# Kernel optimization log

Measured on AMD Instinct MI355X. Metric: run time of the kernel, lower is better.

The kernel has to match this reference:

```python
import jax, jax.numpy as jnp
import numpy as np

BN_EPS = 1e-5

def _bn(x, g, b):
    # BatchNorm1d, training-mode batch statistics
    mu = x.mean(axis=0)
    var = x.var(axis=0)
    return g * (x - mu) / jnp.sqrt(var + BN_EPS) + b

def setup_inputs() -> dict:
    key = jax.random.key(0)
    ks = jax.random.split(key, 10)
    B2, D_in, D1, DIMS, C = 16384, 1024, 512, 256, 40
    B = B2 // 2
    def w(k, shape, fan_in):
        return jax.random.normal(k, shape, jnp.float32) / np.float32(np.sqrt(fan_in))
    return {
        "lufeat": jax.random.normal(ks[0], (B2, D_in), jnp.float32),
        "llabel": jax.random.randint(ks[1], (B,), 0, C),
        "W1": w(ks[2], (D_in, D1), D_in), "b1": jnp.zeros(D1, jnp.float32),
        "W2": w(ks[3], (D1, DIMS), D1), "b2": jnp.zeros(DIMS, jnp.float32),
        "W3": w(ks[4], (DIMS + C, 256), DIMS + C), "b3": jnp.zeros(256, jnp.float32),
        "W4": w(ks[5], (256, 64), 256), "b4": jnp.zeros(64, jnp.float32),
        "W5": w(ks[6], (64, 1), 64), "b5": jnp.zeros(1, jnp.float32),
        "g1": jnp.ones(256, jnp.float32), "be1": jnp.zeros(256, jnp.float32),
        "g2": jnp.ones(64, jnp.float32), "be2": jnp.zeros(64, jnp.float32),
        "mbank0": jax.random.normal(ks[7], (C, DIMS), jnp.float32),
        "start0": jnp.zeros(C, jnp.float32),
    }

def reference(lufeat, llabel, W1, b1, W2, b2, W3, b3, W4, b4, W5, b5,
              g1, be1, g2, be2, mbank0, start0):
    B = lufeat.shape[0] // 2
    h = (lufeat @ W1 + b1) @ W2 + b2            # [2B, dims]
    h = h / jnp.linalg.norm(h, axis=1, keepdims=True)
    lfeat, ufeat = h[:B], h[B:]

    # Sequential per-sample memory-bank scatter/EMA update (detached feats)
    lf_sg = jax.lax.stop_gradient(lfeat)
    def step(carry, xs):
        start, mbank = carry
        lab, feat = xs
        row = jnp.where(start[lab] == 0, feat, 0.9 * mbank[lab] + 0.1 * feat)
        return (start.at[lab].set(1.0), mbank.at[lab].set(row)), None
    (_, mbank), _ = jax.lax.scan(step, (start0, mbank0), (llabel, lf_sg))
    mbank = jax.lax.stop_gradient(mbank)

    # cdist retrieval: [B, C] euclidean distances
    lm = jnp.linalg.norm(lfeat[:, None, :] - mbank[None, :, :], axis=-1)
    lscores = lm.min(axis=-1)
    um = jnp.linalg.norm(ufeat[:, None, :] - mbank[None, :, :], axis=-1)

    uf = jnp.concatenate([ufeat, um], axis=-1)   # [B, dims + C]
    u = jax.nn.relu(_bn(uf @ W3 + b3, g1, be1))
    u = jax.nn.relu(_bn(u @ W4 + b4, g2, be2))   # dropout = identity (eval)
    uscores = u @ W5 + b5                        # [B, 1]
    return lscores, uscores, mbank
```

## Files before the change

kernel.cpp:

```cpp
#include <hip/hip_runtime.h>
#include <hip/hip_bf16.h>
#include <stdint.h>

typedef __attribute__((ext_vector_type(4))) float f32x4;
typedef __attribute__((ext_vector_type(8))) short s16x8;
typedef __attribute__((ext_vector_type(4))) unsigned short u16x4;
typedef __attribute__((ext_vector_type(4))) int i32x4;

#define B2T 16384
#define BH 8192
#define DIN 1024
#define DD1 512
#define DIMS 256
#define NC 40
#define CAPS 2048

__device__ __forceinline__ unsigned short f2b(float f) {
  unsigned int u = __builtin_bit_cast(unsigned int, f);
  u += 0x7FFFu + ((u >> 16) & 1u);
  return (unsigned short)(u >> 16);
}

__global__ __launch_bounds__(256) void prep_weff(const float* __restrict__ W1,
                                                 const float* __restrict__ W2,
                                                 unsigned short* __restrict__ WeffT) {
  __shared__ float W1s[32][33];
  __shared__ float W2s[32][33];
  int t = threadIdx.x;
  int k0 = blockIdx.x * 32, n0 = blockIdx.y * 32;
  int nn = t & 31, kq = t >> 5;
  float acc[4] = {0.f, 0.f, 0.f, 0.f};
  for (int j0 = 0; j0 < DD1; j0 += 32) {
#pragma unroll
    for (int i = 0; i < 4; ++i) {
      int idx = t + 256 * i;
      int kk = idx >> 5, jj = idx & 31;
      W1s[kk][jj] = W1[(size_t)(k0 + kk) * DD1 + j0 + jj];
      W2s[kk][jj] = W2[(size_t)(j0 + kk) * DIMS + n0 + jj];
    }
    __syncthreads();
#pragma unroll
    for (int jj = 0; jj < 32; ++jj) {
      float w2v = W2s[jj][nn];
#pragma unroll
      for (int q = 0; q < 4; ++q) acc[q] += W1s[kq * 4 + q][jj] * w2v;
    }
    __syncthreads();
  }
  u16x4 pk;
#pragma unroll
  for (int q = 0; q < 4; ++q) pk[q] = f2b(acc[q]);
  *(u16x4*)(WeffT + (size_t)(n0 + nn) * DIN + k0 + kq * 4) = pk;
}

__global__ __launch_bounds__(256) void prep_misc(const float* __restrict__ b1,
                                                 const float* __restrict__ W2,
                                                 const float* __restrict__ b2,
                                                 const float* __restrict__ W3,
                                                 const float* __restrict__ W4,
                                                 float* __restrict__ beff,
                                                 unsigned short* __restrict__ W3T,
                                                 unsigned short* __restrict__ W4T) {
  int b = blockIdx.x, t = threadIdx.x;
  if (b == 0) {
    float a0 = 0.f, a1 = 0.f, a2 = 0.f, a3 = 0.f, a4 = 0.f, a5 = 0.f, a6 = 0.f, a7 = 0.f;
    for (int j = 0; j < DD1; j += 8) {
      a0 += b1[j + 0] * W2[(size_t)(j + 0) * DIMS + t];
      a1 += b1[j + 1] * W2[(size_t)(j + 1) * DIMS + t];
      a2 += b1[j + 2] * W2[(size_t)(j + 2) * DIMS + t];
      a3 += b1[j + 3] * W2[(size_t)(j + 3) * DIMS + t];
      a4 += b1[j + 4] * W2[(size_t)(j + 4) * DIMS + t];
      a5 += b1[j + 5] * W2[(size_t)(j + 5) * DIMS + t];
      a6 += b1[j + 6] * W2[(size_t)(j + 6) * DIMS + t];
      a7 += b1[j + 7] * W2[(size_t)(j + 7) * DIMS + t];
    }
    beff[t] = b2[t] + (((a0 + a1) + (a2 + a3)) + ((a4 + a5) + (a6 + a7)));
  } else if (b <= 320) {
    int idx = (b - 1) * 256 + t;
    int n = idx / 320, k = idx - n * 320;
    float v = (k < 296) ? W3[(size_t)k * 256 + n] : 0.0f;
    W3T[(size_t)n * 320 + k] = f2b(v);
  } else {
    int idx = (b - 321) * 256 + t;
    int n = idx >> 8, k = idx & 255;
    W4T[(size_t)n * 256 + k] = f2b(W4[(size_t)k * 64 + n]);
  }
}

template <int AMODE, int NB, int MI, int CW, int EPI>
__global__ __launch_bounds__(256) void gemm_core(
    const void* __restrict__ Aptr, int lda, const unsigned short* __restrict__ BT,
    const float* __restrict__ bias, float* __restrict__ C, int ldc, int K,
    float* __restrict__ sums, float* __restrict__ ssqs,
    const float* __restrict__ bnsum, const float* __restrict__ bnssq,
    const float* __restrict__ bng, const float* __restrict__ bnbe,
    unsigned short* __restrict__ uf) {
  constexpr int AR = (4 / CW) * MI * 16;
  __shared__ short A_s[AR][72];
  __shared__ short B_s[NB][72];
  __shared__ float rs[4][AR];
  int t = threadIdx.x;
  int m0 = blockIdx.x * AR;
  int w = t >> 6, lane = t & 63, q = lane >> 4, ln = lane & 15;
  f32x4 acc[MI][4];
#pragma unroll
  for (int mi = 0; mi < MI; ++mi)
#pragma unroll
    for (int ni = 0; ni < 4; ++ni) acc[mi][ni] = (f32x4){0.f, 0.f, 0.f, 0.f};

  for (int kk = 0; kk < K; kk += 64) {
    if constexpr (AMODE == 0 || AMODE == 2) {
      const float* A = (const float*)Aptr;
#pragma unroll
      for (int i = 0; i < AR / 32; ++i) {
        int ch = t + 256 * i;
        int row = ch >> 3, kp = (ch & 7) * 8;
        const f32x4* src = (const f32x4*)(A + (size_t)(m0 + row) * lda + kk + kp);
        f32x4 v0 = src[0], v1 = src[1];
        if constexpr (AMODE == 2) {
          float vv[8] = {v0[0], v0[1], v0[2], v0[3], v1[0], v1[1], v1[2], v1[3]};
#pragma unroll
          for (int j = 0; j < 8; ++j) {
            int f = kk + kp + j;
            float mu = bnsum[f] * (1.0f / 8192.0f);
            float var = bnssq[f] * (1.0f / 8192.0f) - mu * mu;
            float sc = bng[f] * rsqrtf(var + 1e-5f);
            float sh = bnbe[f] - mu * sc;
            vv[j] = fmaxf(vv[j] * sc + sh, 0.0f);
          }
          v0 = (f32x4){vv[0], vv[1], vv[2], vv[3]};
          v1 = (f32x4){vv[4], vv[5], vv[6], vv[7]};
        }
        s16x8 p;
        p[0] = (short)f2b(v0[0]); p[1] = (short)f2b(v0[1]);
        p[2] = (short)f2b(v0[2]); p[3] = (short)f2b(v0[3]);
        p[4] = (short)f2b(v1[0]); p[5] = (short)f2b(v1[1]);
        p[6] = (short)f2b(v1[2]); p[7] = (short)f2b(v1[3]);
        *(s16x8*)&A_s[row][kp] = p;
      }
    } else {
      const unsigned short* A = (const unsigned short*)Aptr;
#pragma unroll
      for (int i = 0; i < AR / 32; ++i) {
        int ch = t + 256 * i;
        int row = ch >> 3, kp = (ch & 7) * 8;
        *(s16x8*)&A_s[row][kp] = *(const s16x8*)(A + (size_t)(m0 + row) * lda + kk + kp);
      }
    }
#pragma unroll
    for (int i = 0; i < NB * 8 / 256; ++i) {
      int ch = t + 256 * i;
      int n = ch >> 3, kp = (ch & 7) * 8;
      *(s16x8*)&B_s[n][kp] = *(const s16x8*)(BT + (size_t)n * K + kk + kp);
    }
    __syncthreads();
#pragma unroll
    for (int k32 = 0; k32 < 64; k32 += 32) {
      s16x8 af[MI];
      int ab = (w / CW) * MI * 16;
#pragma unroll
      for (int mi = 0; mi < MI; ++mi)
        af[mi] = *(const s16x8*)&A_s[ab + mi * 16 + ln][k32 + q * 8];
      int nb0 = (w % CW) * 64;
#pragma unroll
      for (int ni = 0; ni < 4; ++ni) {
        s16x8 bfr = *(const s16x8*)&B_s[nb0 + ni * 16 + ln][k32 + q * 8];
#pragma unroll
        for (int mi = 0; mi < MI; ++mi)
          acc[mi][ni] = __builtin_amdgcn_mfma_f32_16x16x32_bf16(af[mi], bfr, acc[mi][ni], 0, 0, 0);
      }
    }
    __syncthreads();
  }

  float v[MI][4][4];
#pragma unroll
  for (int mi = 0; mi < MI; ++mi)
#pragma unroll
    for (int ni = 0; ni < 4; ++ni) {
      float bv = bias[(w % CW) * 64 + ni * 16 + ln];
#pragma unroll
      for (int r = 0; r < 4; ++r) v[mi][ni][r] = acc[mi][ni][r] + bv;
    }

  if constexpr (EPI == 1) {
    float p[MI][4];
#pragma unroll
    for (int mi = 0; mi < MI; ++mi)
#pragma unroll
      for (int r = 0; r < 4; ++r) {
        float s = v[mi][0][r] * v[mi][0][r] + v[mi][1][r] * v[mi][1][r] +
                  v[mi][2][r] * v[mi][2][r] + v[mi][3][r] * v[mi][3][r];
        s += __shfl_xor(s, 1); s += __shfl_xor(s, 2);
        s += __shfl_xor(s, 4); s += __shfl_xor(s, 8);
        p[mi][r] = s;
      }
    if (ln == 0) {
#pragma unroll
      for (int mi = 0; mi < MI; ++mi)
#pragma unroll
        for (int r = 0; r < 4; ++r) rs[w][mi * 16 + q * 4 + r] = p[mi][r];
    }
    __syncthreads();
    if (t < AR) rs[0][t] = rsqrtf(rs[0][t] + rs[1][t] + rs[2][t] + rs[3][t]);
    __syncthreads();
#pragma unroll
    for (int mi = 0; mi < MI; ++mi)
#pragma unroll
      for (int r = 0; r < 4; ++r) {
        int rib = mi * 16 + q * 4 + r;
        float inv = rs[0][rib];
        int grow = m0 + rib;
#pragma unroll
        for (int ni = 0; ni < 4; ++ni) {
          int col = w * 64 + ni * 16 + ln;
          float nv = v[mi][ni][r] * inv;
          C[(size_t)grow * ldc + col] = nv;
          if (grow >= BH) uf[(size_t)(grow - BH) * 320 + col] = f2b(nv);
        }
      }
  } else {
#pragma unroll
    for (int mi = 0; mi < MI; ++mi)
#pragma unroll
      for (int ni = 0; ni < 4; ++ni)
#pragma unroll
        for (int r = 0; r < 4; ++r) {
          int grow = m0 + (w / CW) * MI * 16 + mi * 16 + q * 4 + r;
          int col = (w % CW) * 64 + ni * 16 + ln;
          C[(size_t)grow * ldc + col] = v[mi][ni][r];
        }
    if constexpr (EPI == 2 || EPI == 3) {
#pragma unroll
      for (int ni = 0; ni < 4; ++ni) {
        float s = 0.f, s2 = 0.f;
#pragma unroll
        for (int mi = 0; mi < MI; ++mi)
#pragma unroll
          for (int r = 0; r < 4; ++r) {
            float x = v[mi][ni][r];
            s += x; s2 += x * x;
          }
        s += __shfl_xor(s, 16); s += __shfl_xor(s, 32);
        s2 += __shfl_xor(s2, 16); s2 += __shfl_xor(s2, 32);
        if (q == 0) {
          int col = (w % CW) * 64 + ni * 16 + ln;
          atomicAdd(&sums[col], s);
          atomicAdd(&ssqs[col], s2);
        }
      }
    }
  }
}

__global__ __launch_bounds__(256) void bank_kernel(const int* __restrict__ llabel,
                                                   const float* __restrict__ Hn,
                                                   const float* __restrict__ mbank0,
                                                   const float* __restrict__ start0,
                                                   float* __restrict__ mbank_out,
                                                   float* __restrict__ msq) {
  __shared__ i32x4 lab4[BH / 4];
  __shared__ int idx_s[CAPS];
  __shared__ int wcnt[4];
  __shared__ float red[4];
  int t = threadIdx.x, c = blockIdx.x;
  int w = t >> 6, lane = t & 63;

  for (int i = t; i < BH / 4; i += 256) lab4[i] = ((const i32x4*)llabel)[i];
  __syncthreads();
  const int* lab_s = (const int*)lab4;

  int base0 = w * (BH / 4);
  int cnt = 0;
  for (int b = 0; b < BH / 4; b += 64)
    cnt += (int)__popcll(__ballot(lab_s[base0 + b + lane] == c));
  if (lane == 0) wcnt[w] = cnt;
  __syncthreads();
  int off = 0;
#pragma unroll
  for (int i = 0; i < 4; ++i)
    if (i < w) off += wcnt[i];
  int Ktot = wcnt[0] + wcnt[1] + wcnt[2] + wcnt[3];

  int running = off;
  for (int b = 0; b < BH / 4; b += 64) {
    bool hit = lab_s[base0 + b + lane] == c;
    unsigned long long mk = __ballot(hit);
    if (hit) {
      int pos = running + (int)__popcll(mk & ((1ull << lane) - 1ull));
      if (pos < CAPS) idx_s[pos] = base0 + b + lane;
    }
    running += (int)__popcll(mk);
  }
  __syncthreads();
  int K = Ktot < CAPS ? Ktot : CAPS;

  const float l09 = -0.15200309344504997f;
  bool fresh = (start0[c] == 0.0f);
  float out;
  if (K == 0) {
    out = mbank0[(size_t)c * DIMS + t];
  } else {
    float a0 = 0.f, a1 = 0.f, a2 = 0.f, a3 = 0.f, a4 = 0.f, a5 = 0.f, a6 = 0.f, a7 = 0.f;
    float w0fold = fresh ? exp2f((float)K * l09) : 0.f;
    int m = 0;
    for (; m + 8 <= K; m += 8) {
      float e = (float)(K - 1 - m);
      float wa = 0.1f * exp2f(e * l09) + (m == 0 ? w0fold : 0.f);
      a0 += wa * Hn[(size_t)idx_s[m + 0] * DIMS + t];
      a1 += 0.1f * exp2f((e - 1.f) * l09) * Hn[(size_t)idx_s[m + 1] * DIMS + t];
      a2 += 0.1f * exp2f((e - 2.f) * l09) * Hn[(size_t)idx_s[m + 2] * DIMS + t];
      a3 += 0.1f * exp2f((e - 3.f) * l09) * Hn[(size_t)idx_s[m + 3] * DIMS + t];
      a4 += 0.1f * exp2f((e - 4.f) * l09) * Hn[(size_t)idx_s[m + 4] * DIMS + t];
      a5 += 0.1f * exp2f((e - 5.f) * l09) * Hn[(size_t)idx_s[m + 5] * DIMS + t];
      a6 += 0.1f * exp2f((e - 6.f) * l09) * Hn[(size_t)idx_s[m + 6] * DIMS + t];
      a7 += 0.1f * exp2f((e - 7.f) * l09) * Hn[(size_t)idx_s[m + 7] * DIMS + t];
    }
    for (; m < K; ++m) {
      float wa = 0.1f * exp2f((float)(K - 1 - m) * l09) + (m == 0 ? w0fold : 0.f);
      a0 += wa * Hn[(size_t)idx_s[m] * DIMS + t];
    }
    float acc = ((a0 + a1) + (a2 + a3)) + ((a4 + a5) + (a6 + a7));
    float base_v = fresh ? 0.f : exp2f((float)K * l09) * mbank0[(size_t)c * DIMS + t];
    out = acc + base_v;
  }
  mbank_out[(size_t)c * DIMS + t] = out;
  float vv = out * out;
#pragma unroll
  for (int o = 32; o; o >>= 1) vv += __shfl_xor(vv, o);
  if ((t & 63) == 0) red[t >> 6] = vv;
  __syncthreads();
  if (t == 0) msq[c] = (red[0] + red[1]) + (red[2] + red[3]);
}

__global__ __launch_bounds__(128) void dist_kernel(const float* __restrict__ Hn,
                                                   const float* __restrict__ mbank,
                                                   const float* __restrict__ msq,
                                                   float* __restrict__ lscores,
                                                   unsigned short* __restrict__ uf) {
  __shared__ float Ms[NC][260];
  __shared__ float Hs[16][260];
  __shared__ float msq_s[NC];
  int t = threadIdx.x;
  int r0 = blockIdx.x * 16;
  for (int i = 0; i < NC; ++i) {
    Ms[i][t] = mbank[(size_t)i * DIMS + t];
    Ms[i][t + 128] = mbank[(size_t)i * DIMS + t + 128];
  }
  for (int i = 0; i < 16; ++i) {
    Hs[i][t] = Hn[(size_t)(r0 + i) * DIMS + t];
    Hs[i][t + 128] = Hn[(size_t)(r0 + i) * DIMS + t + 128];
  }
  if (t < NC) msq_s[t] = msq[t];
  __syncthreads();
  int r = t >> 3, c0 = (t & 7) * 5;
  float g0 = 0, g1 = 0, g2 = 0, g3 = 0, g4 = 0;
  for (int d = 0; d < DIMS; d += 4) {
    f32x4 f = *(const f32x4*)&Hs[r][d];
    f32x4 m0v = *(const f32x4*)&Ms[c0 + 0][d];
    f32x4 m1v = *(const f32x4*)&Ms[c0 + 1][d];
    f32x4 m2v = *(const f32x4*)&Ms[c0 + 2][d];
    f32x4 m3v = *(const f32x4*)&Ms[c0 + 3][d];
    f32x4 m4v = *(const f32x4*)&Ms[c0 + 4][d];
    g0 += f[0] * m0v[0] + f[1] * m0v[1] + f[2] * m0v[2] + f[3] * m0v[3];
    g1 += f[0] * m1v[0] + f[1] * m1v[1] + f[2] * m1v[2] + f[3] * m1v[3];
    g2 += f[0] * m2v[0] + f[1] * m2v[1] + f[2] * m2v[2] + f[3] * m2v[3];
    g3 += f[0] * m3v[0] + f[1] * m3v[1] + f[2] * m3v[2] + f[3] * m3v[3];
    g4 += f[0] * m4v[0] + f[1] * m4v[1] + f[2] * m4v[2] + f[3] * m4v[3];
  }
  int row = r0 + r;
  float d2[5];
  d2[0] = 1.0f + msq_s[c0 + 0] - 2.0f * g0;
  d2[1] = 1.0f + msq_s[c0 + 1] - 2.0f * g1;
  d2[2] = 1.0f + msq_s[c0 + 2] - 2.0f * g2;
  d2[3] = 1.0f + msq_s[c0 + 3] - 2.0f * g3;
  d2[4] = 1.0f + msq_s[c0 + 4] - 2.0f * g4;
  if (row < BH) {
    float mn = fminf(fminf(fminf(d2[0], d2[1]), fminf(d2[2], d2[3])), d2[4]);
    mn = fminf(mn, __shfl_xor(mn, 1, 8));
    mn = fminf(mn, __shfl_xor(mn, 2, 8));
    mn = fminf(mn, __shfl_xor(mn, 4, 8));
    if ((t & 7) == 0) lscores[row] = sqrtf(fmaxf(mn, 0.0f));
  } else {
    unsigned short* dst = uf + (size_t)(row - BH) * 320 + 256 + c0;
#pragma unroll
    for (int qq = 0; qq < 5; ++qq) dst[qq] = f2b(sqrtf(fmaxf(d2[qq], 0.0f)));
  }
}

__global__ __launch_bounds__(256) void uscore_bn(const float* __restrict__ y2,
                                                 const float* __restrict__ sums2,
                                                 const float* __restrict__ ssqs2,
                                                 const float* __restrict__ g2,
                                                 const float* __restrict__ be2,
                                                 const float* __restrict__ W5,
                                                 const float* __restrict__ b5,
                                                 float* __restrict__ out) {
  int t = threadIdx.x;
  int wv = t >> 6, lane = t & 63;
  int row = blockIdx.x * 4 + wv;
  float mu = sums2[lane] * (1.0f / 8192.0f);
  float var = ssqs2[lane] * (1.0f / 8192.0f) - mu * mu;
  float sc = g2[lane] * rsqrtf(var + 1e-5f);
  float sh = be2[lane] - mu * sc;
  float v = fmaxf(y2[(size_t)row * 64 + lane] * sc + sh, 0.0f) * W5[lane];
#pragma unroll
  for (int o = 32; o; o >>= 1) v += __shfl_xor(v, o);
  if (lane == 0) out[row] = v + b5[0];
}

extern "C" void kernel_launch(void* const* d_in, const int* in_sizes, int n_in,
                              void* d_out, int out_size, void* d_ws, size_t ws_size,
                              hipStream_t stream) {
  const float* lufeat = (const float*)d_in[0];
  const int* llabel = (const int*)d_in[1];
  const float* W1 = (const float*)d_in[2];
  const float* b1 = (const float*)d_in[3];
  const float* W2 = (const float*)d_in[4];
  const float* b2 = (const float*)d_in[5];
  const float* W3 = (const float*)d_in[6];
  const float* b3 = (const float*)d_in[7];
  const float* W4 = (const float*)d_in[8];
  const float* b4 = (const float*)d_in[9];
  const float* W5 = (const float*)d_in[10];
  const float* b5 = (const float*)d_in[11];
  const float* g1 = (const float*)d_in[12];
  const float* be1 = (const float*)d_in[13];
  const float* g2 = (const float*)d_in[14];
  const float* be2 = (const float*)d_in[15];
  const float* mbank0 = (const float*)d_in[16];
  const float* start0 = (const float*)d_in[17];

  char* ws = (char*)d_ws;
  unsigned short* WeffT = (unsigned short*)(ws + 0);
  float* Hraw = (float*)(ws + 524288);
  float* ybuf = (float*)(ws + 524288);
  float* y2 = (float*)(ws + 8912896);
  unsigned short* uf = (unsigned short*)(ws + 17301504);
  unsigned short* W3T = (unsigned short*)(ws + 22544384);
  unsigned short* W4T = (unsigned short*)(ws + 22708224);
  float* beff = (float*)(ws + 22740992);
  float* sums1 = (float*)(ws + 22742016);
  float* ssq1 = sums1 + 256;
  float* sums2 = ssq1 + 256;
  float* ssq2 = sums2 + 64;
  float* msq = (float*)(ws + 22744576);

  float* lscores = (float*)d_out;
  float* uscores = lscores + 8192;
  float* mbank = uscores + 8192;

  hipMemsetAsync(sums1, 0, (256 + 256 + 64 + 64) * sizeof(float), stream);

  prep_weff<<<dim3(32, 8), 256, 0, stream>>>(W1, W2, WeffT);
  prep_misc<<<385, 256, 0, stream>>>(b1, W2, b2, W3, W4, beff, W3T, W4T);
  gemm_core<0, 256, 2, 4, 1><<<512, 256, 0, stream>>>(
      lufeat, 1024, WeffT, beff, Hraw, 256, 1024,
      nullptr, nullptr, nullptr, nullptr, nullptr, nullptr, uf);
  bank_kernel<<<NC, 256, 0, stream>>>(llabel, Hraw, mbank0, start0, mbank, msq);
  dist_kernel<<<1024, 128, 0, stream>>>(Hraw, mbank, msq, lscores, uf);
  gemm_core<1, 256, 2, 4, 2><<<256, 256, 0, stream>>>(
      uf, 320, W3T, b3, ybuf, 256, 320,
      sums1, ssq1, nullptr, nullptr, nullptr, nullptr, nullptr);
  gemm_core<2, 64, 1, 1, 3><<<128, 256, 0, stream>>>(
      ybuf, 256, W4T, b4, y2, 64, 256,
      sums2, ssq2, sums1, ssq1, g1, be1, nullptr);
  uscore_bn<<<2048, 256, 0, stream>>>(y2, sums2, ssq2, g2, be2, W5, b5, uscores);
}
```

Before: 264.2 us.

## Merge prep kernels and memset into one launch; double dist_kernel rows per block

Folds prep_weff, prep_misc and the stats memset into a single prep_all launch, which removes two launches and a memset. The W1·W2 product now stores W2 transposed in shared memory so the inner loop can use float4 LDS reads. dist_kernel switches to 256 threads handling 32 rows per block, which halves the grid and spreads the mbank staging over more rows. The visible compute indexing (r = t>>3) may need matching changes in the hidden part of the kernel.

New measurement: 244.4 us. -7.5%, faster.

```diff
diff --git a/kernel.cpp b/kernel.cpp
--- a/kernel.cpp
+++ b/kernel.cpp
@@ -21,48 +21,50 @@
   return (unsigned short)(u >> 16);
 }
 
-__global__ __launch_bounds__(256) void prep_weff(const float* __restrict__ W1,
-                                                 const float* __restrict__ W2,
-                                                 unsigned short* __restrict__ WeffT) {
-  __shared__ float W1s[32][33];
-  __shared__ float W2s[32][33];
-  int t = threadIdx.x;
-  int k0 = blockIdx.x * 32, n0 = blockIdx.y * 32;
-  int nn = t & 31, kq = t >> 5;
-  float acc[4] = {0.f, 0.f, 0.f, 0.f};
-  for (int j0 = 0; j0 < DD1; j0 += 32) {
-#pragma unroll
-    for (int i = 0; i < 4; ++i) {
-      int idx = t + 256 * i;
-      int kk = idx >> 5, jj = idx & 31;
-      W1s[kk][jj] = W1[(size_t)(k0 + kk) * DD1 + j0 + jj];
-      W2s[kk][jj] = W2[(size_t)(j0 + kk) * DIMS + n0 + jj];
-    }
-    __syncthreads();
-#pragma unroll
-    for (int jj = 0; jj < 32; ++jj) {
-      float w2v = W2s[jj][nn];
-#pragma unroll
-      for (int q = 0; q < 4; ++q) acc[q] += W1s[kq * 4 + q][jj] * w2v;
-    }
-    __syncthreads();
-  }
-  u16x4 pk;
-#pragma unroll
-  for (int q = 0; q < 4; ++q) pk[q] = f2b(acc[q]);
-  *(u16x4*)(WeffT + (size_t)(n0 + nn) * DIN + k0 + kq * 4) = pk;
-}
-
-__global__ __launch_bounds__(256) void prep_misc(const float* __restrict__ b1,
-                                                 const float* __restrict__ W2,
-                                                 const float* __restrict__ b2,
-                                                 const float* __restrict__ W3,
-                                                 const float* __restrict__ W4,
-                                                 float* __restrict__ beff,
-                                                 unsigned short* __restrict__ W3T,
-                                                 unsigned short* __restrict__ W4T) {
+__global__ __launch_bounds__(256) void prep_all(const float* __restrict__ W1,
+                                                const float* __restrict__ W2,
+                                                const float* __restrict__ b1,
+                                                const float* __restrict__ b2,
+                                                const float* __restrict__ W3,
+                                                const float* __restrict__ W4,
+                                                unsigned short* __restrict__ WeffT,
+                                                float* __restrict__ beff,
+                                                unsigned short* __restrict__ W3T,
+                                                unsigned short* __restrict__ W4T,
+                                                float* __restrict__ statz) {
+  __shared__ float W1s[32][36];
+  __shared__ float W2sT[32][36];
   int b = blockIdx.x, t = threadIdx.x;
-  if (b == 0) {
+  if (b < 256) {
+    int k0 = (b & 31) * 32, n0 = (b >> 5) * 32;
+    int nn = t & 31, kq = t >> 5;
+    f32x4 acc = (f32x4){0.f, 0.f, 0.f, 0.f};
+    for (int j0 = 0; j0 < DD1; j0 += 32) {
+#pragma unroll
+      for (int i = 0; i < 4; ++i) {
+        int idx = t + 256 * i;
+        int kk = idx >> 5, jj = idx & 31;
+        W1s[kk][jj] = W1[(size_t)(k0 + kk) * DD1 + j0 + jj];
+        W2sT[jj][kk] = W2[(size_t)(j0 + kk) * DIMS + n0 + jj];
+      }
+      __syncthreads();
+#pragma unroll
+      for (int jj4 = 0; jj4 < 8; ++jj4) {
+        f32x4 w2 = *(const f32x4*)&W2sT[nn][jj4 * 4];
+        f32x4 w1_0 = *(const f32x4*)&W1s[kq * 4 + 0][jj4 * 4];
+        f32x4 w1_1 = *(const f32x4*)&W1s[kq * 4 + 1][jj4 * 4];
+        f32x4 w1_2 = *(const f32x4*)&W1s[kq * 4 + 2][jj4 * 4];
+        f32x4 w1_3 = *(const f32x4*)&W1s[kq * 4 + 3][jj4 * 4];
+        acc[0] += w1_0[0] * w2[0] + w1_0[1] * w2[1] + w1_0[2] * w2[2] + w1_0[3] * w2[3];
+        acc[1] += w1_1[0] * w2[0] + w1_1[1] * w2[1] + w1_1[2] * w2[2] + w1_1[3] * w2[3];
+        acc[2] += w1_2[0] * w2[0] + w1_2[1] * w2[1] + w1_2[2] * w2[2] + w1_2[3] * w2[3];
+        acc[3] += w1_3[0] * w2[0] + w1_3[1] * w2[1] + w1_3[2] * w2[2] + w1_3[3] * w2[3];
+      }
+      __syncthreads();
+    }
+    u16x4 pk = {f2b(acc[0]), f2b(acc[1]), f2b(acc[2]), f2b(acc[3])};
+    *(u16x4*)(WeffT + (size_t)(n0 + nn) * DIN + k0 + kq * 4) = pk;
+  } else if (b == 256) {
     float a0 = 0.f, a1 = 0.f, a2 = 0.f, a3 = 0.f, a4 = 0.f, a5 = 0.f, a6 = 0.f, a7 = 0.f;
     for (int j = 0; j < DD1; j += 8) {
       a0 += b1[j + 0] * W2[(size_t)(j + 0) * DIMS + t];
@@ -75,15 +77,17 @@
       a7 += b1[j + 7] * W2[(size_t)(j + 7) * DIMS + t];
     }
     beff[t] = b2[t] + (((a0 + a1) + (a2 + a3)) + ((a4 + a5) + (a6 + a7)));
-  } else if (b <= 320) {
-    int idx = (b - 1) * 256 + t;
+  } else if (b < 577) {
+    int idx = (b - 257) * 256 + t;
     int n = idx / 320, k = idx - n * 320;
     float v = (k < 296) ? W3[(size_t)k * 256 + n] : 0.0f;
     W3T[(size_t)n * 320 + k] = f2b(v);
-  } else {
-    int idx = (b - 321) * 256 + t;
+  } else if (b < 641) {
+    int idx = (b - 577) * 256 + t;
     int n = idx >> 8, k = idx & 255;
     W4T[(size_t)n * 256 + k] = f2b(W4[(size_t)k * 64 + n]);
+  } else {
+    for (int i = t; i < 640; i += 256) statz[i] = 0.0f;
   }
 }
 
@@ -333,23 +337,23 @@
   if (t == 0) msq[c] = (red[0] + red[1]) + (red[2] + red[3]);
 }
 
-__global__ __launch_bounds__(128) void dist_kernel(const float* __restrict__ Hn,
+__global__ __launch_bounds__(256) void dist_kernel(const float* __restrict__ Hn,
                                                    const float* __restrict__ mbank,
                                                    const float* __restrict__ msq,
                                                    float* __restrict__ lscores,
                                                    unsigned short* __restrict__ uf) {
   __shared__ float Ms[NC][260];
-  __shared__ float Hs[16][260];
+  __shared__ float Hs[32][260];
   __shared__ float msq_s[NC];
   int t = threadIdx.x;
-  int r0 = blockIdx.x * 16;
-  for (int i = 0; i < NC; ++i) {
-    Ms[i][t] = mbank[(size_t)i * DIMS + t];
-    Ms[i][t + 128] = mbank[(size_t)i * DIMS + t + 128];
-  }
-  for (int i = 0; i < 16; ++i) {
-    Hs[i][t] = Hn[(size_t)(r0 + i) * DIMS + t];
-    Hs[i][t + 128] = Hn[(size_t)(r0 + i) * DIMS + t + 128];
+  int r0 = blockIdx.x * 32;
+  for (int e = t; e < NC * 256; e += 256) {
+    int i = e >> 8, d = e & 255;
+    Ms[i][d] = mbank[(size_t)i * DIMS + d];
+  }
+  for (int e = t; e < 32 * 256; e += 256) {
+    int i = e >> 8, d = e & 255;
+    Hs[i][d] = Hn[(size_t)(r0 + i) * DIMS + d];
   }
   if (t < NC) msq_s[t] = msq[t];
   __syncthreads();
@@ -450,15 +454,12 @@
   float* uscores = lscores + 8192;
   float* mbank = uscores + 8192;
 
-  hipMemsetAsync(sums1, 0, (256 + 256 + 64 + 64) * sizeof(float), stream);
-
-  prep_weff<<<dim3(32, 8), 256, 0, stream>>>(W1, W2, WeffT);
-  prep_misc<<<385, 256, 0, stream>>>(b1, W2, b2, W3, W4, beff, W3T, W4T);
+  prep_all<<<642, 256, 0, stream>>>(W1, W2, b1, b2, W3, W4, WeffT, beff, W3T, W4T, sums1);
   gemm_core<0, 256, 2, 4, 1><<<512, 256, 0, stream>>>(
       lufeat, 1024, WeffT, beff, Hraw, 256, 1024,
       nullptr, nullptr, nullptr, nullptr, nullptr, nullptr, uf);
   bank_kernel<<<NC, 256, 0, stream>>>(llabel, Hraw, mbank0, start0, mbank, msq);
-  dist_kernel<<<1024, 128, 0, stream>>>(Hraw, mbank, msq, lscores, uf);
+  dist_kernel<<<512, 256, 0, stream>>>(Hraw, mbank, msq, lscores, uf);
   gemm_core<1, 256, 2, 4, 2><<<256, 256, 0, stream>>>(
       uf, 320, W3T, b3, ybuf, 256, 320,
       sums1, ssq1, nullptr, nullptr, nullptr, nullptr, nullptr);
```
